# Kernel optimization log

Hardware: AMD Instinct MI355X
Metric: run time of the kernel (lower is better)

The kernel has to match this reference:

```python
import jax, jax.numpy as jnp
import numpy as np

EMBED_DIM = 1024
NUM_HEADS = 16
D_K = EMBED_DIM // NUM_HEADS
SCALE = D_K ** -0.5
WEIGHT_EPS = 1e-5


def setup_inputs() -> dict:
    key = jax.random.key(0)
    ks = jax.random.split(key, 12)
    B, T, E = 4, 1024, EMBED_DIM
    init = 1.0 / np.sqrt(E)  # ~ nn.Linear default scale
    inp = {
        "q": jax.random.normal(ks[0], (B, T, E), jnp.float32),
        "k": jax.random.normal(ks[1], (B, T, E), jnp.float32),
        "v": jax.random.normal(ks[2], (B, T, E), jnp.float32),
        "weights": jax.random.uniform(ks[3], (B, T), jnp.float32),
        "Wq": jax.random.uniform(ks[4], (E, E), jnp.float32, -init, init),
        "bq": jax.random.uniform(ks[5], (E,), jnp.float32, -init, init),
        "Wk": jax.random.uniform(ks[6], (E, E), jnp.float32, -init, init),
        "bk": jax.random.uniform(ks[7], (E,), jnp.float32, -init, init),
        "Wv": jax.random.uniform(ks[8], (E, E), jnp.float32, -init, init),
        "bv": jax.random.uniform(ks[9], (E,), jnp.float32, -init, init),
        "Wo": jax.random.uniform(ks[10], (E, E), jnp.float32, -init, init),
        "bo": jax.random.uniform(ks[11], (E,), jnp.float32, -init, init),
    }
    return inp


def reference(q, k, v, weights, Wq, bq, Wk, bk, Wv, bv, Wo, bo):
    B, T, E = q.shape
    H, Dk = NUM_HEADS, D_K
    # linear projections (torch Linear: x @ W.T + b), split into heads
    qh = (q @ Wq.T + bq).reshape(B, T, H, Dk).transpose(0, 2, 1, 3)  # [B,H,T,Dk]
    kh = (k @ Wk.T + bk).reshape(B, T, H, Dk).transpose(0, 2, 1, 3)
    vh = (v @ Wv.T + bv).reshape(B, T, H, Dk).transpose(0, 2, 1, 3)
    # scaled energy [B,H,Tq,Tk]
    energy = jnp.einsum("bhqd,bhkd->bhqk", qh, kh) * SCALE
    # weight^2 gating over key axis + masked_fill(-inf) where weight < eps
    w = weights[:, None, None, :]  # [B,1,1,Tk]
    energy = jnp.where(w < WEIGHT_EPS, -jnp.inf, energy * (w * w))
    attn = jax.nn.softmax(energy, axis=-1)  # dropout is identity in eval mode
    out = jnp.einsum("bhqk,bhkd->bhqd", attn, vh)  # [B,H,T,Dk]
    out = out.transpose(0, 2, 1, 3).reshape(B, T, E)
    return out @ Wo.T + bo
```

## Files before the change

kernel.cpp:

```cpp
#include <hip/hip_runtime.h>
#include <hip/hip_bf16.h>
#include <stdint.h>

using frag = __attribute__((ext_vector_type(8))) short;
using f4   = __attribute__((ext_vector_type(4))) float;
using bf16 = __hip_bfloat16;

static constexpr float WEPS = 1e-5f;
static constexpr float SC2K  = 0.125f * 1.44269504f;
static constexpr float EBIAS = -8.0f * 1.44269504f;

#define AS1(p) ((const __attribute__((address_space(1))) void*)(p))
#define AS3(p) ((__attribute__((address_space(3))) void*)(p))

__device__ __forceinline__ void gl2lds16(const void* g, void* l) {
    __builtin_amdgcn_global_load_lds(AS1(g), AS3(l), 16, 0, 0);
}

__device__ inline uint4 pack8(float4 a, float4 b) {
    union { bf16 h[8]; uint4 u; } x;
    x.h[0] = __float2bfloat16(a.x); x.h[1] = __float2bfloat16(a.y);
    x.h[2] = __float2bfloat16(a.z); x.h[3] = __float2bfloat16(a.w);
    x.h[4] = __float2bfloat16(b.x); x.h[5] = __float2bfloat16(b.y);
    x.h[6] = __float2bfloat16(b.z); x.h[7] = __float2bfloat16(b.w);
    return x.u;
}

__device__ __forceinline__ uint2 pack4(float a, float b, float c, float d) {
    union { bf16 h[4]; uint2 u; } x;
    x.h[0] = __float2bfloat16(a); x.h[1] = __float2bfloat16(b);
    x.h[2] = __float2bfloat16(c); x.h[3] = __float2bfloat16(d);
    return x.u;
}

__device__ __forceinline__ int tperm(int t) {
    return (t & ~63) | (((t & 15) << 2) | ((t >> 4) & 3));
}

struct CvtArgs {
    const float* src[7];
    long long    bounds[8];
    long long    total;
};

__global__ __launch_bounds__(256) void cvt_kernel(CvtArgs a, bf16* __restrict__ dst)
{
    long long e = ((long long)blockIdx.x * 256 + threadIdx.x) * 8;
    if (e >= a.total) return;
    int s = 0;
    while (e >= a.bounds[s + 1]) s++;
    const float* src = a.src[s] + (e - a.bounds[s]);
    float4 f0 = ((const float4*)src)[0];
    float4 f1 = ((const float4*)src)[1];
    *(uint4*)(dst + e) = pack8(f0, f1);
}

struct GemmBatch {
    const void*  A[3];
    const void*  W[3];
    const float* bias[3];
    void*        Out[3];
    int          mode[3];
};

template<bool ABF, bool WBF>
__global__ __launch_bounds__(256) void gemm_batch(GemmBatch g)
{
    constexpr int K = 1024;
    __shared__ bf16 As[2][128 * 32];
    __shared__ bf16 Bs[2][128 * 32];

    const int z = blockIdx.z;
    const void*  Ap   = g.A[z];
    const void*  Wp   = g.W[z];
    const float* bias = g.bias[z];
    void*        OutP = g.Out[z];
    const int    mode = g.mode[z];

    const int tid = threadIdx.x;
    const int lid = blockIdx.x + 8 * blockIdx.y;
    const int big   = (lid & 7) * 4 + (lid >> 6);
    const int small = (lid >> 3) & 7;
    int m0, n0;
    if (mode == 4) { m0 = small * 128; n0 = big * 128; }
    else           { m0 = big * 128;   n0 = small * 128; }

    const int lane = tid & 63;
    const int wave = tid >> 6;
    const int wm   = (wave >> 1) * 64;
    const int wn   = (wave & 1) * 64;
    const int lr   = lane & 15;
    const int q    = lane >> 4;

    const int sr = tid >> 1;
    const int sc = (tid & 1) * 16;

    const int c0 = wave * 128 + lane;
    const int c1 = c0 + 64;
    const int r0 = c0 >> 2, col0 = (c0 & 3) * 8;
    const int r1 = c1 >> 2, col1 = (c1 & 3) * 8;

    auto stage = [&](int k0, int pb) {
        if (WBF) {
            const bf16* W = (const bf16*)Wp;
            gl2lds16(&W[(size_t)(n0 + r0) * K + k0 + col0], &Bs[pb][wave * 1024]);
            gl2lds16(&W[(size_t)(n0 + r1) * K + k0 + col1], &Bs[pb][wave * 1024 + 512]);
        } else {
            const float* W = (const float*)Wp;
            const float* src = &W[(size_t)(n0 + sr) * K + k0 + sc];
            float4 f0 = ((const float4*)src)[0];
            float4 f1 = ((const float4*)src)[1];
            float4 f2 = ((const float4*)src)[2];
            float4 f3 = ((const float4*)src)[3];
            *(uint4*)(&Bs[pb][sr * 32 + sc])     = pack8(f0, f1);
            *(uint4*)(&Bs[pb][sr * 32 + sc + 8]) = pack8(f2, f3);
        }
        if (ABF) {
            const bf16* A = (const bf16*)Ap;
            gl2lds16(&A[(size_t)(m0 + r0) * K + k0 + col0], &As[pb][wave * 1024]);
            gl2lds16(&A[(size_t)(m0 + r1) * K + k0 + col1], &As[pb][wave * 1024 + 512]);
        } else {
            const float* A = (const float*)Ap;
            const float* src = &A[(size_t)(m0 + sr) * K + k0 + sc];
            float4 f0 = ((const float4*)src)[0];
            float4 f1 = ((const float4*)src)[1];
            float4 f2 = ((const float4*)src)[2];
            float4 f3 = ((const float4*)src)[3];
            *(uint4*)(&As[pb][sr * 32 + sc])     = pack8(f0, f1);
            *(uint4*)(&As[pb][sr * 32 + sc + 8]) = pack8(f2, f3);
        }
    };

    f4 acc[4][4];
    #pragma unroll
    for (int i = 0; i < 4; i++)
        #pragma unroll
        for (int j = 0; j < 4; j++) acc[i][j] = f4{0.f, 0.f, 0.f, 0.f};

    stage(0, 0);
    __syncthreads();

    for (int kt = 0; kt < 32; kt++) {
        const int cb = kt & 1;
        if (kt < 31) stage((kt + 1) * 32, cb ^ 1);

        frag af[4], bfr[4];
        #pragma unroll
        for (int i = 0; i < 4; i++)
            af[i] = *(const frag*)(&As[cb][(wm + i * 16 + lr) * 32 + q * 8]);
        #pragma unroll
        for (int j = 0; j < 4; j++)
            bfr[j] = *(const frag*)(&Bs[cb][(wn + j * 16 + lr) * 32 + q * 8]);
        #pragma unroll
        for (int i = 0; i < 4; i++)
            #pragma unroll
            for (int j = 0; j < 4; j++)
                acc[i][j] = __builtin_amdgcn_mfma_f32_16x16x32_bf16(af[i], bfr[j], acc[i][j], 0, 0, 0);
        __syncthreads();
    }

    if (mode == 4) {
        const int bbt   = (n0 + wn) >> 10;
        const int tbase = (n0 + wn) & 1023;
        bf16* O = (bf16*)OutP;
        #pragma unroll
        for (int i = 0; i < 4; i++) {
            int row0 = m0 + wm + i * 16 + q * 4;
            #pragma unroll
            for (int r = 0; r < 4; r++) {
                int f = row0 + r;
                int h = f >> 6, d = f & 63;
                float bv = bias[f];
                size_t idx = ((((size_t)bbt * 16 + h) * 64 + d) << 10) + tbase + lr * 4;
                *(uint2*)(&O[idx]) = pack4(acc[i][0][r] + bv, acc[i][1][r] + bv,
                                           acc[i][2][r] + bv, acc[i][3][r] + bv);
            }
        }
    } else {
        #pragma unroll
        for (int i = 0; i < 4; i++) {
            int row0 = m0 + wm + i * 16 + q * 4;
            #pragma unroll
            for (int j = 0; j < 4; j++) {
                int col = n0 + wn + j * 16 + lr;
                float bv = bias[col];
                #pragma unroll
                for (int r = 0; r < 4; r++) {
                    float val = acc[i][j][r] + bv;
                    int mrow = row0 + r;
                    if (mode == 3) {
                        ((float*)OutP)[(size_t)mrow * 1024 + col] = val;
                    } else {
                        int bb = mrow >> 10, t = mrow & 1023;
                        int h  = col >> 6,   d = col & 63;
                        size_t idx;
                        if (mode == 2)
                            idx = ((((size_t)bb * 16 + h) * 64 + d) << 10) + tperm(t);
                        else
                            idx = ((((size_t)bb * 16 + h) << 10) + t) * 64 + d;
                        ((bf16*)OutP)[idx] = __float2bfloat16(val);
                    }
                }
            }
        }
    }
}

template<bool WBF>
__global__ __launch_bounds__(256) void gemm_out(const bf16* __restrict__ A,
                                                const void* __restrict__ Wp,
                                                const float* __restrict__ bias,
                                                float* __restrict__ Out)
{
    constexpr int K = 1024;
    __shared__ bf16 As[2][64 * 64];
    __shared__ bf16 Bs[2][128 * 64];

    const int tid = threadIdx.x;
    const int lid = blockIdx.x + 8 * blockIdx.y;
    const int mt  = (lid & 7) * 8 + (lid >> 6);
    const int nt  = (lid >> 3) & 7;
    const int n0  = nt * 128;
    const int m0  = mt * 64;
    const int lane = tid & 63;
    const int wave = tid >> 6;
    const int wm   = (wave >> 1) * 32;
    const int wn   = (wave & 1) * 64;
    const int lr   = lane & 15;
    const int q    = lane >> 4;

    const int sr = tid >> 1;
    const int sc = (tid & 1) * 32;

    int rb[4], cb4[4];
    #pragma unroll
    for (int gg = 0; gg < 4; gg++) {
        int D = wave * 256 + gg * 64 + lane;
        rb[gg]  = D >> 3;
        cb4[gg] = (D & 7) * 8;
    }
    int ra[2], ca4[2];
    #pragma unroll
    for (int gg = 0; gg < 2; gg++) {
        int D = wave * 128 + gg * 64 + lane;
        ra[gg]  = D >> 3;
        ca4[gg] = (D & 7) * 8;
    }

    auto stage = [&](int k0, int pb) {
        if (WBF) {
            const bf16* W = (const bf16*)Wp;
            #pragma unroll
            for (int gg = 0; gg < 4; gg++)
                gl2lds16(&W[(size_t)(n0 + rb[gg]) * K + k0 + cb4[gg]],
                         &Bs[pb][(wave * 256 + gg * 64) * 8]);
        } else {
            const float* W = (const float*)Wp;
            const float* src = &W[(size_t)(n0 + sr) * K + k0 + sc];
            #pragma unroll
            for (int c = 0; c < 4; c++) {
                float4 f0 = ((const float4*)src)[2 * c];
                float4 f1 = ((const float4*)src)[2 * c + 1];
                *(uint4*)(&Bs[pb][sr * 64 + sc + c * 8]) = pack8(f0, f1);
            }
        }
        #pragma unroll
        for (int gg = 0; gg < 2; gg++)
            gl2lds16(&A[(size_t)(m0 + ra[gg]) * K + k0 + ca4[gg]],
                     &As[pb][(wave * 128 + gg * 64) * 8]);
    };

    f4 acc[2][4];
    #pragma unroll
    for (int i = 0; i < 2; i++)
        #pragma unroll
        for (int j = 0; j < 4; j++) acc[i][j] = f4{0.f, 0.f, 0.f, 0.f};

    stage(0, 0);
    __syncthreads();

    for (int kt = 0; kt < 16; kt++) {
        const int cb = kt & 1;
        if (kt < 15) stage((kt + 1) * 64, cb ^ 1);

        #pragma unroll
        for (int kk = 0; kk < 2; kk++) {
            frag af[2], bfr[4];
            #pragma unroll
            for (int i = 0; i < 2; i++)
                af[i] = *(const frag*)(&As[cb][(wm + i * 16 + lr) * 64 + kk * 32 + q * 8]);
            #pragma unroll
            for (int j = 0; j < 4; j++)
                bfr[j] = *(const frag*)(&Bs[cb][(wn + j * 16 + lr) * 64 + kk * 32 + q * 8]);
            #pragma unroll
            for (int i = 0; i < 2; i++)
                #pragma unroll
                for (int j = 0; j < 4; j++)
                    acc[i][j] = __builtin_amdgcn_mfma_f32_16x16x32_bf16(af[i], bfr[j], acc[i][j], 0, 0, 0);
        }
        __syncthreads();
    }

    #pragma unroll
    for (int i = 0; i < 2; i++) {
        int row0 = m0 + wm + i * 16 + q * 4;
        #pragma unroll
        for (int j = 0; j < 4; j++) {
            int col = n0 + wn + j * 16 + lr;
            float bv = bias[col];
            #pragma unroll
            for (int r = 0; r < 4; r++)
                Out[(size_t)(row0 + r) * 1024 + col] = acc[i][j][r] + bv;
        }
    }
}

__global__ __launch_bounds__(256, 3) void attn_kernel(const bf16* __restrict__ qh,
                                                      const bf16* __restrict__ kh,
                                                      const bf16* __restrict__ vhT,
                                                      const float* __restrict__ wts,
                                                      bf16* __restrict__ att)
{
    constexpr int LDP = 72;
    __shared__ bf16 Ks[2][64 * 64];
    __shared__ bf16 Vs[2][64 * 64];
    __shared__ bf16 Plds[4][32 * LDP];

    const int tid  = threadIdx.x;
    const int lane = tid & 63;
    const int wave = tid >> 6;
    const int lr   = lane & 15;
    const int q    = lane >> 4;
    const int bh   = blockIdx.x;
    const int bb   = bh >> 4;
    const int h    = bh & 15;
    const int q0w  = blockIdx.y * 128 + wave * 32;
    const size_t base = (size_t)bh * 1024 * 64;

    const int cA = wave * 128 + lane;
    const int cB = cA + 64;
    const int rowA = cA >> 3, gA = ((cA & 7) ^ (rowA & 7)) * 8;
    const int rowB = cB >> 3, gB = ((cB & 7) ^ (rowB & 7)) * 8;

    frag aq[2][2];
    #pragma unroll
    for (int rf = 0; rf < 2; rf++)
        #pragma unroll
        for (int ks = 0; ks < 2; ks++)
            aq[rf][ks] = *(const frag*)(&qh[base + (size_t)(q0w + rf * 16 + lr) * 64 + ks * 32 + q * 8]);

    float rs[2][4];
    f4 o[2][4];
    #pragma unroll
    for (int rf = 0; rf < 2; rf++)
        #pragma unroll
        for (int j = 0; j < 4; j++) {
            o[rf][j] = f4{0.f, 0.f, 0.f, 0.f};
            rs[rf][j] = 0.f;
        }

    gl2lds16(&kh [base + (size_t)rowA * 64 + gA],   &Ks[0][wave * 1024]);
    gl2lds16(&kh [base + (size_t)rowB * 64 + gB],   &Ks[0][wave * 1024 + 512]);
    gl2lds16(&vhT[base + (size_t)rowA * 1024 + gA], &Vs[0][wave * 1024]);
    gl2lds16(&vhT[base + (size_t)rowB * 1024 + gB], &Vs[0][wave * 1024 + 512]);
    __syncthreads();

    for (int t = 0; t < 16; t++) {
        const int k0  = t * 64;
        const int buf = t & 1;
        if (t < 15) {
            int kn = k0 + 64;
            gl2lds16(&kh [base + (size_t)(kn + rowA) * 64 + gA],  &Ks[buf ^ 1][wave * 1024]);
            gl2lds16(&kh [base + (size_t)(kn + rowB) * 64 + gB],  &Ks[buf ^ 1][wave * 1024 + 512]);
            gl2lds16(&vhT[base + (size_t)rowA * 1024 + kn + gA], &Vs[buf ^ 1][wave * 1024]);
            gl2lds16(&vhT[base + (size_t)rowB * 1024 + kn + gB], &Vs[buf ^ 1][wave * 1024 + 512]);
        }

        float sc2[4], eb[4];
        #pragma unroll
        for (int j = 0; j < 4; j++) {
            float w = wts[bb * 1024 + k0 + j * 16 + lr];
            sc2[j] = SC2K * w * w;
            eb[j]  = (w < WEPS) ? -1e30f : EBIAS;
        }

        frag kb[4][2];
        #pragma unroll
        for (int j = 0; j < 4; j++) {
            int rowj = j * 16 + lr;
            kb[j][0] = *(const frag*)(&Ks[buf][rowj * 64 + (((q    ) ^ (rowj & 7)) * 8)]);
            kb[j][1] = *(const frag*)(&Ks[buf][rowj * 64 + (((q + 4) ^ (rowj & 7)) * 8)]);
        }

        #pragma unroll
        for (int rf = 0; rf < 2; rf++) {
            f4 s[4];
            #pragma unroll
            for (int j = 0; j < 4; j++) {
                f4 z = f4{0.f, 0.f, 0.f, 0.f};
                s[j] = __builtin_amdgcn_mfma_f32_16x16x32_bf16(aq[rf][0], kb[j][0], z, 0, 0, 0);
                s[j] = __builtin_amdgcn_mfma_f32_16x16x32_bf16(aq[rf][1], kb[j][1], s[j], 0, 0, 0);
            }
            float p[4][4];
            #pragma unroll
            for (int j = 0; j < 4; j++)
                #pragma unroll
                for (int r = 0; r < 4; r++) {
                    p[j][r] = __builtin_amdgcn_exp2f(fmaf(s[j][r], sc2[j], eb[j]));
                    rs[rf][r] += p[j][r];
                }
            #pragma unroll
            for (int r = 0; r < 4; r++)
                *(uint2*)(&Plds[wave][(rf * 16 + q * 4 + r) * LDP + lr * 4]) =
                    pack4(p[0][r], p[1][r], p[2][r], p[3][r]);
        }

        frag vb[4][2];
        #pragma unroll
        for (int j = 0; j < 4; j++) {
            int rowj = j * 16 + lr;
            vb[j][0] = *(const frag*)(&Vs[buf][rowj * 64 + (((q    ) ^ (rowj & 7)) * 8)]);
            vb[j][1] = *(const frag*)(&Vs[buf][rowj * 64 + (((q + 4) ^ (rowj & 7)) * 8)]);
        }

        #pragma unroll
        for (int rf = 0; rf < 2; rf++) {
            frag ap0 = *(const frag*)(&Plds[wave][(rf * 16 + lr) * LDP + q * 8]);
            frag ap1 = *(const frag*)(&Plds[wave][(rf * 16 + lr) * LDP + 32 + q * 8]);
            #pragma unroll
            for (int j = 0; j < 4; j++) {
                o[rf][j] = __builtin_amdgcn_mfma_f32_16x16x32_bf16(ap0, vb[j][0], o[rf][j], 0, 0, 0);
                o[rf][j] = __builtin_amdgcn_mfma_f32_16x16x32_bf16(ap1, vb[j][1], o[rf][j], 0, 0, 0);
            }
        }
        __syncthreads();
    }

    #pragma unroll
    for (int off = 1; off < 16; off <<= 1)
        #pragma unroll
        for (int rf = 0; rf < 2; rf++)
            #pragma unroll
            for (int r = 0; r < 4; r++)
                rs[rf][r] += __shfl_xor(rs[rf][r], off, 64);

    #pragma unroll
    for (int rf = 0; rf < 2; rf++) {
        float inv[4];
        #pragma unroll
        for (int r = 0; r < 4; r++) inv[r] = 1.0f / rs[rf][r];
        const int t0 = q0w + rf * 16 + q * 4;
        #pragma unroll
        for (int j = 0; j < 4; j++) {
            int d = h * 64 + j * 16 + lr;
            #pragma unroll
            for (int r = 0; r < 4; r++)
                att[((size_t)bb * 1024 + t0 + r) * 1024 + d] =
                    __float2bfloat16(o[rf][j][r] * inv[r]);
        }
    }
}

extern "C" void kernel_launch(void* const* d_in, const int* in_sizes, int n_in,
                              void* d_out, int out_size, void* d_ws, size_t ws_size,
                              hipStream_t stream)
{
    const float* q   = (const float*)d_in[0];
    const float* k   = (const float*)d_in[1];
    const float* v   = (const float*)d_in[2];
    const float* wts = (const float*)d_in[3];
    const float* Wq  = (const float*)d_in[4];
    const float* bq  = (const float*)d_in[5];
    const float* Wk  = (const float*)d_in[6];
    const float* bk  = (const float*)d_in[7];
    const float* Wv  = (const float*)d_in[8];
    const float* bv  = (const float*)d_in[9];
    const float* Wo  = (const float*)d_in[10];
    const float* bo  = (const float*)d_in[11];
    float* out = (float*)d_out;

    const long long Mi = 1024 * 1024;
    bf16* qh  = (bf16*)d_ws;
    bf16* kh  = qh  + 4 * Mi;
    bf16* vhT = kh  + 4 * Mi;
    bf16* att = vhT + 4 * Mi;
    bf16* cvt = att + 4 * Mi;
    const size_t base_bytes = (size_t)32 * Mi;

    dim3 blk(256);

    if (ws_size >= base_bytes + (size_t)32 * Mi) {
        CvtArgs ca{};
        ca.src[0] = q;  ca.src[1] = k;  ca.src[2] = v;
        ca.src[3] = Wq; ca.src[4] = Wk; ca.src[5] = Wv; ca.src[6] = Wo;
        long long bnd[8] = {0, 4*Mi, 8*Mi, 12*Mi, 13*Mi, 14*Mi, 15*Mi, 16*Mi};
        for (int i = 0; i < 8; i++) ca.bounds[i] = bnd[i];
        ca.total = 16 * Mi;
        cvt_kernel<<<8192, blk, 0, stream>>>(ca, cvt);

        GemmBatch gq{};
        gq.A[0] = cvt;          gq.A[1] = cvt + 4*Mi;   gq.A[2] = cvt + 14*Mi;
        gq.W[0] = cvt + 12*Mi;  gq.W[1] = cvt + 13*Mi;  gq.W[2] = cvt + 8*Mi;
        gq.bias[0] = bq; gq.bias[1] = bk; gq.bias[2] = bv;
        gq.Out[0] = qh;  gq.Out[1] = kh;  gq.Out[2] = vhT;
        gq.mode[0] = 0;  gq.mode[1] = 0;  gq.mode[2] = 4;
        gemm_batch<true, true><<<dim3(8, 32, 3), blk, 0, stream>>>(gq);

        attn_kernel<<<dim3(64, 8), blk, 0, stream>>>(qh, kh, vhT, wts, att);

        gemm_out<true><<<dim3(8, 64), blk, 0, stream>>>(att, cvt + 15*Mi, bo, out);
    } else if (ws_size >= base_bytes + (size_t)8 * Mi) {
        CvtArgs ca{};
        ca.src[0] = Wq; ca.src[1] = Wk; ca.src[2] = Wv; ca.src[3] = Wo;
        long long bnd[8] = {0, 1*Mi, 2*Mi, 3*Mi, 4*Mi, 4*Mi, 4*Mi, 4*Mi};
        for (int i = 0; i < 8; i++) ca.bounds[i] = bnd[i];
        ca.total = 4 * Mi;
        cvt_kernel<<<2048, blk, 0, stream>>>(ca, cvt);

        GemmBatch gq{};
        gq.A[0] = q; gq.A[1] = k; gq.A[2] = v;
        gq.W[0] = cvt; gq.W[1] = cvt + 1*Mi; gq.W[2] = cvt + 2*Mi;
        gq.bias[0] = bq; gq.bias[1] = bk; gq.bias[2] = bv;
        gq.Out[0] = qh;  gq.Out[1] = kh;  gq.Out[2] = vhT;
        gq.mode[0] = 0;  gq.mode[1] = 0;  gq.mode[2] = 2;
        gemm_batch<false, true><<<dim3(8, 32, 3), blk, 0, stream>>>(gq);

        attn_kernel<<<dim3(64, 8), blk, 0, stream>>>(qh, kh, vhT, wts, att);

        gemm_out<true><<<dim3(8, 64), blk, 0, stream>>>(att, cvt + 3*Mi, bo, out);
    } else {
        GemmBatch gq{};
        gq.A[0] = q; gq.A[1] = k; gq.A[2] = v;
        gq.W[0] = Wq; gq.W[1] = Wk; gq.W[2] = Wv;
        gq.bias[0] = bq; gq.bias[1] = bk; gq.bias[2] = bv;
        gq.Out[0] = qh;  gq.Out[1] = kh;  gq.Out[2] = vhT;
        gq.mode[0] = 0;  gq.mode[1] = 0;  gq.mode[2] = 2;
        gemm_batch<false, false><<<dim3(8, 32, 3), blk, 0, stream>>>(gq);

        attn_kernel<<<dim3(64, 8), blk, 0, stream>>>(qh, kh, vhT, wts, att);

        gemm_out<false><<<dim3(8, 64), blk, 0, stream>>>(att, Wo, bo, out);
    }
}
```

Measured before the change: 214.4 us.

## Triple-buffer GEMM LDS staging with partial vmcnt waits instead of full barriers

Both projection GEMM kernels move from double to triple buffering of the LDS tiles, prefetching two k-tiles ahead. When the operands are already bf16 (direct global-to-LDS loads), the full __syncthreads is replaced by a partial s_waitcnt vmcnt plus s_barrier, so only the oldest tile's loads must finish. This is meant to hide global memory latency better. It costs more LDS per block, which may lower occupancy, and the hand-set vmcnt counts must match the exact number of loads issued per stage.

```diff
diff --git a/kernel.cpp b/kernel.cpp
--- a/kernel.cpp
+++ b/kernel.cpp
@@ -67,8 +67,8 @@
 __global__ __launch_bounds__(256) void gemm_batch(GemmBatch g)
 {
     constexpr int K = 1024;
-    __shared__ bf16 As[2][128 * 32];
-    __shared__ bf16 Bs[2][128 * 32];
+    __shared__ bf16 As[3][128 * 32];
+    __shared__ bf16 Bs[3][128 * 32];
 
     const int z = blockIdx.z;
     const void*  Ap   = g.A[z];
@@ -138,11 +138,20 @@
         for (int j = 0; j < 4; j++) acc[i][j] = f4{0.f, 0.f, 0.f, 0.f};
 
     stage(0, 0);
-    __syncthreads();
-
+    stage(32, 1);
+    if (ABF && WBF) {
+        asm volatile("s_waitcnt vmcnt(4)" ::: "memory");
+        __builtin_amdgcn_s_barrier();
+    } else {
+        __syncthreads();
+    }
+
+    int cb = 0;
     for (int kt = 0; kt < 32; kt++) {
-        const int cb = kt & 1;
-        if (kt < 31) stage((kt + 1) * 32, cb ^ 1);
+        if (kt < 30) {
+            int sb = cb + 2; if (sb >= 3) sb -= 3;
+            stage((kt + 2) * 32, sb);
+        }
 
         frag af[4], bfr[4];
         #pragma unroll
@@ -156,7 +165,17 @@
             #pragma unroll
             for (int j = 0; j < 4; j++)
                 acc[i][j] = __builtin_amdgcn_mfma_f32_16x16x32_bf16(af[i], bfr[j], acc[i][j], 0, 0, 0);
-        __syncthreads();
+
+        if (kt < 31) {
+            if (ABF && WBF) {
+                if (kt < 30) asm volatile("s_waitcnt vmcnt(4)" ::: "memory");
+                else         asm volatile("s_waitcnt vmcnt(0)" ::: "memory");
+                __builtin_amdgcn_s_barrier();
+            } else {
+                __syncthreads();
+            }
+        }
+        cb = cb + 1; if (cb == 3) cb = 0;
     }
 
     if (mode == 4) {
@@ -213,8 +232,8 @@
                                                 float* __restrict__ Out)
 {
     constexpr int K = 1024;
-    __shared__ bf16 As[2][64 * 64];
-    __shared__ bf16 Bs[2][128 * 64];
+    __shared__ bf16 As[3][64 * 64];
+    __shared__ bf16 Bs[3][128 * 64];
 
     const int tid = threadIdx.x;
     const int lid = blockIdx.x + 8 * blockIdx.y;
@@ -277,11 +296,20 @@
         for (int j = 0; j < 4; j++) acc[i][j] = f4{0.f, 0.f, 0.f, 0.f};
 
     stage(0, 0);
-    __syncthreads();
-
+    stage(64, 1);
+    if (WBF) {
+        asm volatile("s_waitcnt vmcnt(6)" ::: "memory");
+        __builtin_amdgcn_s_barrier();
+    } else {
+        __syncthreads();
+    }
+
+    int cb = 0;
     for (int kt = 0; kt < 16; kt++) {
-        const int cb = kt & 1;
-        if (kt < 15) stage((kt + 1) * 64, cb ^ 1);
+        if (kt < 14) {
+            int sb = cb + 2; if (sb >= 3) sb -= 3;
+            stage((kt + 2) * 64, sb);
+        }
 
         #pragma unroll
         for (int kk = 0; kk < 2; kk++) {
@@ -298,7 +326,17 @@
                 for (int j = 0; j < 4; j++)
                     acc[i][j] = __builtin_amdgcn_mfma_f32_16x16x32_bf16(af[i], bfr[j], acc[i][j], 0, 0, 0);
         }
-        __syncthreads();
+
+        if (kt < 15) {
+            if (WBF) {
+                if (kt < 14) asm volatile("s_waitcnt vmcnt(6)" ::: "memory");
+                else         asm volatile("s_waitcnt vmcnt(0)" ::: "memory");
+                __builtin_amdgcn_s_barrier();
+            } else {
+                __syncthreads();
+            }
+        }
+        cb = cb + 1; if (cb == 3) cb = 0;
     }
 
     #pragma unroll
```

Result: faster. 209.6 us (-2.2%).

## Triple-buffer output GEMM with explicit vmcnt waits and raise MFMA priority in attention

Applied to the files above, without the earlier changes.

The output-projection GEMM moves from a double-buffered LDS pipeline to three buffers, keeping two stages in flight. For bf16 weights, the full __syncthreads is replaced by an explicit s_waitcnt vmcnt(6) plus s_barrier, so only the older async global-to-LDS loads are waited on. The attention kernel wraps its MFMA sequences in s_setprio to favour matrix issue across waves. The extra buffers raise LDS use to about 72KB per block, which may reduce occupancy, and the hardcoded vmcnt count depends on exactly six loads being issued per stage.

```diff
diff --git a/kernel.cpp b/kernel.cpp
--- a/kernel.cpp
+++ b/kernel.cpp
@@ -213,8 +213,8 @@
                                                 float* __restrict__ Out)
 {
     constexpr int K = 1024;
-    __shared__ bf16 As[2][64 * 64];
-    __shared__ bf16 Bs[2][128 * 64];
+    __shared__ bf16 As0[64 * 64], As1[64 * 64], As2[64 * 64];
+    __shared__ bf16 Bs0[128 * 64], Bs1[128 * 64], Bs2[128 * 64];
 
     const int tid = threadIdx.x;
     const int lid = blockIdx.x + 8 * blockIdx.y;
@@ -247,13 +247,13 @@
         ca4[gg] = (D & 7) * 8;
     }
 
-    auto stage = [&](int k0, int pb) {
+    auto stage = [&](int k0, bf16* Asd, bf16* Bsd) {
         if (WBF) {
             const bf16* W = (const bf16*)Wp;
             #pragma unroll
             for (int gg = 0; gg < 4; gg++)
                 gl2lds16(&W[(size_t)(n0 + rb[gg]) * K + k0 + cb4[gg]],
-                         &Bs[pb][(wave * 256 + gg * 64) * 8]);
+                         &Bsd[(wave * 256 + gg * 64) * 8]);
         } else {
             const float* W = (const float*)Wp;
             const float* src = &W[(size_t)(n0 + sr) * K + k0 + sc];
@@ -261,13 +261,13 @@
             for (int c = 0; c < 4; c++) {
                 float4 f0 = ((const float4*)src)[2 * c];
                 float4 f1 = ((const float4*)src)[2 * c + 1];
-                *(uint4*)(&Bs[pb][sr * 64 + sc + c * 8]) = pack8(f0, f1);
+                *(uint4*)(&Bsd[sr * 64 + sc + c * 8]) = pack8(f0, f1);
             }
         }
         #pragma unroll
         for (int gg = 0; gg < 2; gg++)
             gl2lds16(&A[(size_t)(m0 + ra[gg]) * K + k0 + ca4[gg]],
-                     &As[pb][(wave * 128 + gg * 64) * 8]);
+                     &Asd[(wave * 128 + gg * 64) * 8]);
     };
 
     f4 acc[2][4];
@@ -276,29 +276,84 @@
         #pragma unroll
         for (int j = 0; j < 4; j++) acc[i][j] = f4{0.f, 0.f, 0.f, 0.f};
 
-    stage(0, 0);
-    __syncthreads();
-
-    for (int kt = 0; kt < 16; kt++) {
-        const int cb = kt & 1;
-        if (kt < 15) stage((kt + 1) * 64, cb ^ 1);
-
+    auto compute = [&](const bf16* Asp, const bf16* Bsp) {
         #pragma unroll
         for (int kk = 0; kk < 2; kk++) {
             frag af[2], bfr[4];
             #pragma unroll
             for (int i = 0; i < 2; i++)
-                af[i] = *(const frag*)(&As[cb][(wm + i * 16 + lr) * 64 + kk * 32 + q * 8]);
+                af[i] = *(const frag*)(&Asp[(wm + i * 16 + lr) * 64 + kk * 32 + q * 8]);
             #pragma unroll
             for (int j = 0; j < 4; j++)
-                bfr[j] = *(const frag*)(&Bs[cb][(wn + j * 16 + lr) * 64 + kk * 32 + q * 8]);
+                bfr[j] = *(const frag*)(&Bsp[(wn + j * 16 + lr) * 64 + kk * 32 + q * 8]);
             #pragma unroll
             for (int i = 0; i < 2; i++)
                 #pragma unroll
                 for (int j = 0; j < 4; j++)
                     acc[i][j] = __builtin_amdgcn_mfma_f32_16x16x32_bf16(af[i], bfr[j], acc[i][j], 0, 0, 0);
         }
+    };
+
+    if (WBF) {
+        stage(0,   As0, Bs0);
+        stage(64,  As1, Bs1);
+        asm volatile("s_waitcnt vmcnt(6)" ::: "memory");
+        __builtin_amdgcn_s_barrier();
+
+        for (int m = 0; m < 4; m++) {
+            const int kb = m * 192;
+            stage(kb + 128, As2, Bs2);
+            compute(As0, Bs0);
+            asm volatile("s_waitcnt vmcnt(6)" ::: "memory");
+            __builtin_amdgcn_s_barrier();
+
+            stage(kb + 192, As0, Bs0);
+            compute(As1, Bs1);
+            asm volatile("s_waitcnt vmcnt(6)" ::: "memory");
+            __builtin_amdgcn_s_barrier();
+
+            stage(kb + 256, As1, Bs1);
+            compute(As2, Bs2);
+            asm volatile("s_waitcnt vmcnt(6)" ::: "memory");
+            __builtin_amdgcn_s_barrier();
+        }
+        stage(896, As2, Bs2);
+        compute(As0, Bs0);
+        asm volatile("s_waitcnt vmcnt(6)" ::: "memory");
+        __builtin_amdgcn_s_barrier();
+        stage(960, As0, Bs0);
+        compute(As1, Bs1);
+        asm volatile("s_waitcnt vmcnt(6)" ::: "memory");
+        __builtin_amdgcn_s_barrier();
+        compute(As2, Bs2);
+        asm volatile("s_waitcnt vmcnt(0)" ::: "memory");
+        __builtin_amdgcn_s_barrier();
+        compute(As0, Bs0);
+    } else {
+        stage(0,   As0, Bs0);
+        stage(64,  As1, Bs1);
         __syncthreads();
+        for (int m = 0; m < 4; m++) {
+            const int kb = m * 192;
+            stage(kb + 128, As2, Bs2);
+            compute(As0, Bs0);
+            __syncthreads();
+            stage(kb + 192, As0, Bs0);
+            compute(As1, Bs1);
+            __syncthreads();
+            stage(kb + 256, As1, Bs1);
+            compute(As2, Bs2);
+            __syncthreads();
+        }
+        stage(896, As2, Bs2);
+        compute(As0, Bs0);
+        __syncthreads();
+        stage(960, As0, Bs0);
+        compute(As1, Bs1);
+        __syncthreads();
+        compute(As2, Bs2);
+        __syncthreads();
+        compute(As0, Bs0);
     }
 
     #pragma unroll
@@ -395,12 +450,14 @@
         #pragma unroll
         for (int rf = 0; rf < 2; rf++) {
             f4 s[4];
+            __builtin_amdgcn_s_setprio(1);
             #pragma unroll
             for (int j = 0; j < 4; j++) {
                 f4 z = f4{0.f, 0.f, 0.f, 0.f};
                 s[j] = __builtin_amdgcn_mfma_f32_16x16x32_bf16(aq[rf][0], kb[j][0], z, 0, 0, 0);
                 s[j] = __builtin_amdgcn_mfma_f32_16x16x32_bf16(aq[rf][1], kb[j][1], s[j], 0, 0, 0);
             }
+            __builtin_amdgcn_s_setprio(0);
             float p[4][4];
             #pragma unroll
             for (int j = 0; j < 4; j++)
@@ -427,11 +484,13 @@
         for (int rf = 0; rf < 2; rf++) {
             frag ap0 = *(const frag*)(&Plds[wave][(rf * 16 + lr) * LDP + q * 8]);
             frag ap1 = *(const frag*)(&Plds[wave][(rf * 16 + lr) * LDP + 32 + q * 8]);
+            __builtin_amdgcn_s_setprio(1);
             #pragma unroll
             for (int j = 0; j < 4; j++) {
                 o[rf][j] = __builtin_amdgcn_mfma_f32_16x16x32_bf16(ap0, vb[j][0], o[rf][j], 0, 0, 0);
                 o[rf][j] = __builtin_amdgcn_mfma_f32_16x16x32_bf16(ap1, vb[j][1], o[rf][j], 0, 0, 0);
             }
+            __builtin_amdgcn_s_setprio(0);
         }
         __syncthreads();
     }
```

Result: faster. 207.2 us (median of 2 runs) (-3.4%).
